# Kernel tuning notes

Measured on AMD Instinct MI355X. Metric: run time of the kernel, lower is better.

## Reference

```python
import jax, jax.numpy as jnp
import numpy as np

TOPK = 10
NUM_CLASSES = 80
ALPHA = 1.0
BETA = 6.0
EPS = 1e-9
IOU_EPS = 1e-7
IMG = 640.0


def setup_inputs() -> dict:
    key = jax.random.key(0)
    ks = jax.random.split(key, 8)
    B, N, M, C = 8, 16800, 96, NUM_CLASSES
    pd_scores = jax.random.normal(ks[0], (B, N, C), dtype=jnp.float32)
    # predicted boxes: valid xyxy around random centers
    p_c = jax.random.uniform(ks[1], (B, N, 2), dtype=jnp.float32) * IMG
    p_wh = jax.random.uniform(ks[2], (B, N, 2), dtype=jnp.float32) * (IMG / 8.0) + 1.0
    pd_bboxes = jnp.concatenate([p_c - p_wh / 2, p_c + p_wh / 2], axis=-1)
    anchor_points = jax.random.uniform(ks[3], (N, 2), dtype=jnp.float32) * IMG
    gt_labels = jax.random.randint(ks[4], (B, M, 1), 0, C, dtype=jnp.int32)
    g_c = jax.random.uniform(ks[5], (B, M, 2), dtype=jnp.float32) * IMG
    g_wh = jax.random.uniform(ks[6], (B, M, 2), dtype=jnp.float32) * (IMG / 4.0) + 4.0
    gt_bboxes = jnp.concatenate([g_c - g_wh / 2, g_c + g_wh / 2], axis=-1)
    # first 72 of 96 GT slots valid per image (padding mask)
    mask_gt = jnp.broadcast_to((jnp.arange(M) < 72).astype(jnp.float32)[None, :, None], (B, M, 1))
    return {"pd_scores": pd_scores, "pd_bboxes": pd_bboxes, "anchor_points": anchor_points,
            "gt_labels": gt_labels, "gt_bboxes": gt_bboxes, "mask_gt": mask_gt}


def _bbox_iou(b1, b2):
    # b1: (B,N,1,4), b2: (B,1,M,4) -> (B,N,M)
    ix1 = jnp.maximum(b1[..., 0], b2[..., 0])
    iy1 = jnp.maximum(b1[..., 1], b2[..., 1])
    ix2 = jnp.minimum(b1[..., 2], b2[..., 2])
    iy2 = jnp.minimum(b1[..., 3], b2[..., 3])
    inter = jnp.clip(ix2 - ix1, 0.0) * jnp.clip(iy2 - iy1, 0.0)
    a1 = (b1[..., 2] - b1[..., 0]) * (b1[..., 3] - b1[..., 1])
    a2 = (b2[..., 2] - b2[..., 0]) * (b2[..., 3] - b2[..., 1])
    return inter / (a1 + a2 - inter + IOU_EPS)


def _assign(pd_scores, pd_bboxes, anchor_points, gt_labels, gt_bboxes, mask_gt):
    B, N, C = pd_scores.shape
    M = gt_bboxes.shape[1]
    mg = mask_gt[:, :, 0]                      # (B,M)
    gl = gt_labels[:, :, 0].astype(jnp.int32)  # (B,M)

    # --- anchor centers inside GT boxes -> (B,N,M) ---
    lt = gt_bboxes[:, :, None, :2]             # (B,M,1,2)
    rb = gt_bboxes[:, :, None, 2:]
    ap = anchor_points[None, None, :, :]       # (1,1,N,2)
    deltas = jnp.concatenate([ap - lt, rb - ap], axis=-1)  # (B,M,N,4)
    mask_in_gts = jnp.swapaxes(deltas.min(-1) > EPS, 1, 2).astype(pd_scores.dtype)  # (B,N,M)

    # --- IoU + alignment metric ---
    overlaps = jnp.clip(_bbox_iou(pd_bboxes[:, :, None, :], gt_bboxes[:, None, :, :]), 0.0)  # (B,N,M)
    gl_exp = jnp.broadcast_to(gl[:, None, :], (B, N, M))
    bbox_scores = jnp.take_along_axis(pd_scores, gl_exp, axis=2)  # (B,N,M)
    align = (jax.nn.sigmoid(bbox_scores) ** ALPHA) * (overlaps ** BETA)
    align = align * mg[:, None, :]

    # --- top-k anchors per GT (over anchor axis) ---
    mT = jnp.swapaxes(align, 1, 2)                     # (B,M,N)
    topk_vals, topk_idxs = jax.lax.top_k(mT, min(TOPK, N))
    keep = topk_vals.max(-1, keepdims=True) > EPS       # (B,M,1)
    bi = jnp.arange(B)[:, None, None]
    mi = jnp.arange(M)[None, :, None]
    sel = jnp.zeros((B, M, N), dtype=bool).at[bi, mi, topk_idxs].set(True)
    mask_topk = jnp.swapaxes(sel & keep, 1, 2).astype(pd_scores.dtype)  # (B,N,M)

    mask_pos = mask_in_gts * mask_topk * mg[:, None, :]

    # --- resolve anchors assigned to multiple GTs by max IoU ---
    fg_count = mask_pos.sum(2)                          # (B,N)
    multi = (fg_count[:, :, None] > 1)
    is_max = jax.nn.one_hot(overlaps.argmax(2), M, dtype=overlaps.dtype)
    mask_pos = jnp.where(multi, is_max, mask_pos)
    fg_mask = mask_pos.sum(2) > 0                       # (B,N) bool
    target_gt_idx = mask_pos.argmax(2)                  # (B,N)

    # --- gather targets ---
    target_labels = jnp.take_along_axis(gl, target_gt_idx, axis=1)
    target_labels = jnp.clip(target_labels, 0, C - 1)
    target_bboxes = jnp.take_along_axis(gt_bboxes, target_gt_idx[:, :, None], axis=1)  # (B,N,4)

    # --- normalized alignment metric -> scores (faithful .long() truncation) ---
    max_per_gt = jnp.clip(align.max(1, keepdims=True), EPS)
    norm_align = (align / max_per_gt).max(2) * fg_mask.astype(align.dtype)  # (B,N)
    bi2 = jnp.arange(B)[:, None]
    ni = jnp.arange(N)[None, :]
    assigned = jnp.zeros((B, N, C), dtype=jnp.int32).at[bi2, ni, target_labels].set(
        norm_align.astype(jnp.int32))
    target_scores = jnp.where(fg_mask[:, :, None], assigned.astype(pd_scores.dtype),
                              jnp.zeros((), pd_scores.dtype))
    return target_bboxes, target_scores, fg_mask, target_gt_idx


def reference(pd_scores, pd_bboxes, anchor_points, gt_labels, gt_bboxes, mask_gt):
    return _assign(pd_scores, pd_bboxes, anchor_points, gt_labels, gt_bboxes, mask_gt)
```

## Files before the change

kernel.cpp:

```cpp
#include <hip/hip_runtime.h>
#include <math.h>

#define TOPK_K 10
#define EPS_F 1e-9f
#define IOU_EPS_F 1e-7f
#define CH 128
#define CCH 256
#define MGMAX 32

struct Iou6 { float ov; float ov6; };

__device__ __forceinline__ Iou6 iou_pow6(float px1, float py1, float px2, float py2,
                                         float gx1, float gy1, float gx2, float gy2) {
#pragma clang fp contract(off)
  float ix1 = fmaxf(px1, gx1);
  float iy1 = fmaxf(py1, gy1);
  float ix2 = fminf(px2, gx2);
  float iy2 = fminf(py2, gy2);
  float dw = fmaxf(ix2 - ix1, 0.0f);
  float dh = fmaxf(iy2 - iy1, 0.0f);
  float inter = dw * dh;
  float a1 = (px2 - px1) * (py2 - py1);
  float a2 = (gx2 - gx1) * (gy2 - gy1);
  float den = a1 + a2 - inter + IOU_EPS_F;
  float iou = inter / den;
  float ov = fmaxf(iou, 0.0f);
  float ov2 = ov * ov;
  Iou6 r; r.ov = ov; r.ov6 = ov2 * ov2 * ov2;
  return r;
}

__device__ __forceinline__ float sigmoid_f(float x) {
#pragma clang fp contract(off)
  return 1.0f / (1.0f + expf(-x));
}

__device__ __forceinline__ unsigned long long mk_key(float v, int idx) {
  if (idx < 0) return 0ull;
  unsigned uv = __float_as_uint(v) | 0x80000000u;
  return ((unsigned long long)uv << 32) | (unsigned)(~idx);
}

#define KINSERT(kk)                                                      \
  if ((kk) > kl[9]) {                                                    \
    _Pragma("unroll")                                                    \
    for (int j = 9; j >= 1; --j) {                                       \
      if ((kk) > kl[j - 1])      kl[j] = kl[j - 1];                      \
      else if ((kk) > kl[j])     kl[j] = (kk);                           \
    }                                                                    \
    if ((kk) > kl[0]) kl[0] = (kk);                                      \
  }

#define WAVE_MERGE10()                                                         \
  {                                                                            \
    _Pragma("unroll")                                                          \
    for (int r = 0; r < TOPK_K; ++r) {                                         \
      unsigned long long kmine = kl[0], kw = kl[0];                            \
      _Pragma("unroll")                                                        \
      for (int off = 32; off > 0; off >>= 1) {                                 \
        unsigned long long o = __shfl_xor(kw, off);                            \
        if (o > kw) kw = o;                                                    \
      }                                                                        \
      if (lane == 0) skey[wid * TOPK_K + r] = kw;                              \
      if (kmine == kw && kw != 0ull) {                  \
        _Pragma("unroll")                                                      \
        for (int j = 0; j < TOPK_K - 1; ++j) kl[j] = kl[j + 1];                \
        kl[TOPK_K - 1] = 0ull;                                                 \
      }                                                                        \
    }                                                                          \
  }

#define FINAL_MERGE10()                                                        \
  {                                                                            \
    _Pragma("unroll")                                                          \
    for (int r = 0; r < TOPK_K; ++r) {                                         \
      unsigned long long kmine = kl[0], kw = kl[0];                            \
      _Pragma("unroll")                                                        \
      for (int off = 32; off > 0; off >>= 1) {                                 \
        unsigned long long o = __shfl_xor(kw, off);                            \
        if (o > kw) kw = o;                                                    \
      }                                                                        \
      if (r == 0) maxv = __uint_as_float((unsigned)(kw >> 32) & 0x7fffffffu);  \
      if (r == TOPK_K - 1) {                                                   \
        Tv = __uint_as_float((unsigned)(kw >> 32) & 0x7fffffffu);              \
        Ti = (int)~(unsigned)(kw & 0xffffffffu);                               \
      }                                                                        \
      if (kmine == kw && kw != 0ull) {                                         \
        _Pragma("unroll")                                                      \
        for (int j = 0; j < TOPK_K - 1; ++j) kl[j] = kl[j + 1];                \
        kl[TOPK_K - 1] = 0ull;                                                 \
      }                                                                        \
    }                                                                          \
  }

__launch_bounds__(256)
__global__ void k_zero(int* __restrict__ cnt, int n) {
  for (int i = threadIdx.x; i < n; i += 256) cnt[i] = 0;
}

__launch_bounds__(CCH)
__global__ void k_collect(const float* __restrict__ pd_scores,
                          const float* __restrict__ pd_bboxes,
                          const int*   __restrict__ gt_labels,
                          const float* __restrict__ gt_bboxes,
                          const float* __restrict__ mask_gt,
                          int B, int N, int M, int C, int CAP, int MGS,
                          int*    __restrict__ cnt,
                          float2* __restrict__ lists)
{
  const int b = blockIdx.z;
  const int m0 = blockIdx.y * MGS;
  const int mcount = min(MGS, M - m0);
  const int tid = threadIdx.x;
  const int n = blockIdx.x * CCH + tid;
  const int lane = tid & 63;
  const int wid  = tid >> 6;

  __shared__ float4             sgt[MGMAX];
  __shared__ int                sgl[MGMAX];
  __shared__ int                smg[MGMAX];
  __shared__ unsigned long long sbal[CCH / 64][MGMAX];
  __shared__ int                wbase[CCH / 64][MGMAX];

  if (tid < mcount) {
    sgt[tid] = *(const float4*)(gt_bboxes + (size_t)(b * M + m0 + tid) * 4);
    sgl[tid] = min(max(gt_labels[b * M + m0 + tid], 0), C - 1);
    smg[tid] = (mask_gt[b * M + m0 + tid] > 0.0f) ? 1 : 0;
  }
  __syncthreads();

  float4 p = make_float4(-1.f, -1.f, -2.f, -2.f);
  if (n < N) p = *(const float4*)(pd_bboxes + ((size_t)b * N + n) * 4);

  for (int mi = 0; mi < mcount; ++mi) {
    const float4 g = sgt[mi];
    bool pred = false;
    if (smg[mi]) {
      float ix1 = fmaxf(p.x, g.x), iy1 = fmaxf(p.y, g.y);
      float ix2 = fminf(p.z, g.z), iy2 = fminf(p.w, g.w);
      pred = (ix2 > ix1) && (iy2 > iy1);
    }
    unsigned long long bal = __ballot(pred);
    if (lane == 0) sbal[wid][mi] = bal;
  }
  __syncthreads();

  if (tid < mcount) {
    int t0 = __popcll(sbal[0][tid]), t1 = __popcll(sbal[1][tid]);
    int t2 = __popcll(sbal[2][tid]), t3 = __popcll(sbal[3][tid]);
    int tot = t0 + t1 + t2 + t3;
    int gb = (tot > 0) ? atomicAdd(&cnt[b * M + m0 + tid], tot) : 0;
    wbase[0][tid] = gb;
    wbase[1][tid] = gb + t0;
    wbase[2][tid] = gb + t0 + t1;
    wbase[3][tid] = gb + t0 + t1 + t2;
  }
  __syncthreads();

  const float* __restrict__ srow = pd_scores + ((size_t)b * N + n) * C;
  const unsigned long long ltm = (1ull << lane) - 1ull;
  for (int mi = 0; mi < mcount; ++mi) {
    unsigned long long bal = sbal[wid][mi];
    if (bal == 0ull) continue;
    if ((bal >> lane) & 1ull) {
      int pos = wbase[wid][mi] + __popcll(bal & ltm);
      if ((unsigned)pos < (unsigned)CAP) {
        const float4 g = sgt[mi];
        Iou6 io = iou_pow6(p.x, p.y, p.z, p.w, g.x, g.y, g.z, g.w);
        float a = sigmoid_f(srow[sgl[mi]]) * io.ov6;
        lists[(size_t)(b * M + m0 + mi) * CAP + pos] = make_float2(a, __int_as_float(n));
      }
    }
  }
}

__launch_bounds__(256)
__global__ void k_select(const float* __restrict__ pd_scores,
                         const float* __restrict__ pd_bboxes,
                         const int*   __restrict__ gt_labels,
                         const float* __restrict__ gt_bboxes,
                         const float* __restrict__ mask_gt,
                         int B, int N, int M, int C, int CAP,
                         const int*    __restrict__ cnt,
                         const float2* __restrict__ lists,
                         float* __restrict__ maxv_out,
                         float* __restrict__ t10v_out,
                         int*   __restrict__ t10i_out)
{
  const int m = blockIdx.x, b = blockIdx.y;
  const int bm = b * M + m;
  const int tid = threadIdx.x;
  const int lane = tid & 63;
  const int wid  = tid >> 6;

  __shared__ unsigned long long skey[4 * TOPK_K];
  __shared__ int sfb;

  if (mask_gt[bm] == 0.0f) {
    if (tid == 0) { maxv_out[bm] = 0.0f; t10v_out[bm] = 0.0f; t10i_out[bm] = -1; }
    return;
  }

  unsigned long long kl[TOPK_K];
#pragma unroll
  for (int j = 0; j < TOPK_K; ++j) kl[j] = 0ull;

  float maxv = 0.0f, Tv = 0.0f; int Ti = -1;
  const int c = cnt[bm];
  bool fb = (c < TOPK_K) || (c > CAP);

  if (!fb) {
    const float2* __restrict__ lp = lists + (size_t)bm * CAP;
    for (int i = tid; i < c; i += 256) {
      float2 e = lp[i];
      unsigned long long k = mk_key(e.x, __float_as_int(e.y));
      KINSERT(k);
    }
    WAVE_MERGE10();
    __syncthreads();
    if (wid == 0) {
#pragma unroll
      for (int j = 0; j < TOPK_K; ++j) kl[j] = 0ull;
      kl[0] = (lane < 4 * TOPK_K) ? skey[lane] : 0ull;
      FINAL_MERGE10();
      if (lane == 0) sfb = (Tv == 0.0f) ? 1 : 0;
    }
    __syncthreads();
    fb = (sfb != 0);
  }

  if (fb) {
#pragma unroll
    for (int j = 0; j < TOPK_K; ++j) kl[j] = 0ull;
    const float4 g = *(const float4*)(gt_bboxes + (size_t)bm * 4);
    int gl = min(max(gt_labels[bm], 0), C - 1);
    const float* __restrict__ srow = pd_scores + (size_t)b * N * C;
    const float4* __restrict__ pb = (const float4*)(pd_bboxes + (size_t)b * N * 4);
    for (int n = tid; n < N; n += 256) {
      float4 p = pb[n];
      Iou6 io = iou_pow6(p.x, p.y, p.z, p.w, g.x, g.y, g.z, g.w);
      unsigned long long kub = mk_key(io.ov6, 0);
      if (kub > kl[TOPK_K - 1]) {
        float a = (io.ov6 == 0.0f) ? 0.0f
                                   : sigmoid_f(srow[(size_t)n * C + gl]) * io.ov6;
        unsigned long long k = mk_key(a, n);
        KINSERT(k);
      }
    }
    __syncthreads();
    WAVE_MERGE10();
    __syncthreads();
    if (wid == 0) {
#pragma unroll
      for (int j = 0; j < TOPK_K; ++j) kl[j] = 0ull;
      kl[0] = (lane < 4 * TOPK_K) ? skey[lane] : 0ull;
      FINAL_MERGE10();
    }
  }

  if (tid == 0) { maxv_out[bm] = maxv; t10v_out[bm] = Tv; t10i_out[bm] = Ti; }
}

__launch_bounds__(256)
__global__ void k_assign(const float* __restrict__ pd_scores,
                         const float* __restrict__ pd_bboxes,
                         const float* __restrict__ anchors,
                         const int*   __restrict__ gt_labels,
                         const float* __restrict__ gt_bboxes,
                         const float* __restrict__ mask_gt,
                         const float* __restrict__ maxv_in,
                         const float* __restrict__ t10v_in,
                         const int*   __restrict__ t10i_in,
                         int B, int N, int M, int C,
                         float* __restrict__ out)
{
  const int b = blockIdx.y;
  const int chunk0 = blockIdx.x * CH;
  const int tid = threadIdx.x;
  const int al   = tid & (CH - 1);
  const int half = tid >> 7;
  const int n = chunk0 + al;

  __shared__ float4 sgt[128];
  __shared__ int    sgl[128];
  __shared__ float  smg[128];
  __shared__ float  smpg[128];
  __shared__ float  spre[128];
  __shared__ float  smT[128];
  __shared__ int    smI[128];
  __shared__ int    skeep[128];
  __shared__ float  s_pov[CH];
  __shared__ int    s_parg[CH], s_pcnt[CH], s_pfirst[CH], s_pone[CH];
  __shared__ int    slab[CH];
  __shared__ float  ssv[CH];

  if (tid < M) {
    sgt[tid] = *(const float4*)(gt_bboxes + (size_t)(b * M + tid) * 4);
    sgl[tid] = min(max(gt_labels[b * M + tid], 0), C - 1);
    smg[tid] = mask_gt[b * M + tid];
    float mv  = maxv_in[b * M + tid];
    float mpg = fmaxf(mv, EPS_F);
    smpg[tid] = mpg;
    spre[tid] = mpg * 0.999999f;
    smT[tid]  = t10v_in[b * M + tid];
    smI[tid]  = t10i_in[b * M + tid];
    skeep[tid] = (mv > EPS_F) ? 1 : 0;
  }
  __syncthreads();

  float* __restrict__ out_bbox   = out;
  float* __restrict__ out_scores = out + (size_t)B * N * 4;
  float* __restrict__ out_fg     = out_scores + (size_t)B * N * C;
  float* __restrict__ out_tgt    = out_fg + (size_t)B * N;

  const bool valid = (n < N);
  float pov = -1.0f; int parg = 0;
  int pcnt = 0, pfirst = -1, pone = 0;

  if (valid) {
    const float4 p = *(const float4*)(pd_bboxes + ((size_t)b * N + n) * 4);
    const float ax = anchors[(size_t)n * 2];
    const float ay = anchors[(size_t)n * 2 + 1];
    const float* __restrict__ srow = pd_scores + ((size_t)b * N + n) * C;

    const int mhalf = (M + 1) >> 1;
    const int mlo = half ? mhalf : 0;
    const int mhi = half ? M : mhalf;

    for (int m = mlo; m < mhi; ++m) {
      const float4 gbb = sgt[m];
      Iou6 io = iou_pow6(p.x, p.y, p.z, p.w, gbb.x, gbb.y, gbb.z, gbb.w);
      if (io.ov > pov) { pov = io.ov; parg = m; }
      const float mgv = smg[m];
      if (mgv > 0.0f) {
        const float T = smT[m];
        const int keep = skeep[m];
        bool mem = false;
        const bool cand = keep && (io.ov6 > T);
        if (cand || (io.ov6 >= spre[m])) {
          const float a = sigmoid_f(srow[sgl[m]]) * io.ov6;
          if (cand) mem = (a > T) || (a == T && n <= smI[m]);
          if (a / smpg[m] >= 1.0f) pone = 1;
        } else if (keep && (T == 0.0f) && (io.ov6 == 0.0f)) {
          mem = (n <= smI[m]);
        }
        if (mem) {
          const float d = fminf(fminf(ax - gbb.x, ay - gbb.y),
                                fminf(gbb.z - ax, gbb.w - ay));
          if (d > EPS_F) { pcnt++; if (pfirst < 0) pfirst = m; }
        }
      }
    }
  }

  if (half == 1 && valid) {
    s_pov[al] = pov; s_parg[al] = parg; s_pcnt[al] = pcnt;
    s_pfirst[al] = pfirst; s_pone[al] = pone;
  }
  __syncthreads();

  if (half == 0 && valid) {
    float ov1 = s_pov[al];
    if (ov1 > pov) { pov = ov1; parg = s_parg[al]; }
    pcnt += s_pcnt[al];
    if (pfirst < 0) pfirst = s_pfirst[al];
    pone |= s_pone[al];

    float fg; int tgt;
    if (pcnt > 1)       { fg = 1.0f; tgt = parg; }
    else if (pcnt == 1) { fg = 1.0f; tgt = pfirst; }
    else                { fg = 0.0f; tgt = 0; }

    slab[al] = sgl[tgt];
    ssv[al]  = (fg > 0.0f && pone) ? 1.0f : 0.0f;

    *(float4*)(out_bbox + ((size_t)b * N + n) * 4) = sgt[tgt];
    out_fg[(size_t)b * N + n]  = fg;
    out_tgt[(size_t)b * N + n] = (float)tgt;
  }
  __syncthreads();

  const int rows = min(CH, N - chunk0);
  const int c4n = C >> 2;
  float4* __restrict__ os4 = (float4*)(out_scores + ((size_t)b * N + chunk0) * C);
  const int tot = rows * c4n;
  if (c4n == 20) {
    for (int i = tid; i < tot; i += 256) {
      unsigned row = __umulhi((unsigned)i, 0xCCCCCCCDu) >> 4;
      int c0 = (i - (int)row * 20) * 4;
      int lr = slab[row]; float v = ssv[row];
      float4 o;
      o.x = (c0     == lr) ? v : 0.0f;
      o.y = (c0 + 1 == lr) ? v : 0.0f;
      o.z = (c0 + 2 == lr) ? v : 0.0f;
      o.w = (c0 + 3 == lr) ? v : 0.0f;
      os4[i] = o;
    }
  } else {
    for (int i = tid; i < tot; i += 256) {
      int row = i / c4n;
      int c0 = (i - row * c4n) * 4;
      int lr = slab[row]; float v = ssv[row];
      float4 o;
      o.x = (c0     == lr) ? v : 0.0f;
      o.y = (c0 + 1 == lr) ? v : 0.0f;
      o.z = (c0 + 2 == lr) ? v : 0.0f;
      o.w = (c0 + 3 == lr) ? v : 0.0f;
      os4[i] = o;
    }
  }
}

extern "C" void kernel_launch(void* const* d_in, const int* in_sizes, int n_in,
                              void* d_out, int out_size, void* d_ws, size_t ws_size,
                              hipStream_t stream) {
  const float* pd_scores = (const float*)d_in[0];
  const float* pd_bboxes = (const float*)d_in[1];
  const float* anchors   = (const float*)d_in[2];
  const int*   gt_labels = (const int*)d_in[3];
  const float* gt_bboxes = (const float*)d_in[4];
  const float* mask_gt   = (const float*)d_in[5];

  const int N = in_sizes[2] / 2;
  const int B = in_sizes[1] / (N * 4);
  const int M = in_sizes[3] / B;
  const int C = in_sizes[0] / (B * N);
  const int BM = B * M;

  char* ws = (char*)d_ws;
  float*  maxv  = (float*)ws;  ws += (size_t)BM * 4;
  float*  t10v  = (float*)ws;  ws += (size_t)BM * 4;
  int*    t10i  = (int*)ws;    ws += (size_t)BM * 4;
  int*    cnt   = (int*)ws;    ws += (size_t)BM * 4;
  float2* lists = (float2*)ws;

  const size_t header = (size_t)BM * 16;
  size_t avail = (ws_size > header) ? (ws_size - header) : 0;
  long long capll = (long long)(avail / ((size_t)BM * 8));
  int CAP = (int)((capll > 4096) ? 4096 : capll);
  if (CAP < 512) CAP = 0;

  k_zero<<<1, 256, 0, stream>>>(cnt, BM);

  if (CAP > 0) {
    int MGRP = 8;
    int MGS  = (M + MGRP - 1) / MGRP;
    while (MGS > MGMAX) { MGRP *= 2; MGS = (M + MGRP - 1) / MGRP; }
    dim3 gc((N + CCH - 1) / CCH, MGRP, B);
    k_collect<<<gc, CCH, 0, stream>>>(pd_scores, pd_bboxes, gt_labels, gt_bboxes,
                                      mask_gt, B, N, M, C, CAP, MGS, cnt, lists);
  }

  dim3 gs(M, B);
  k_select<<<gs, 256, 0, stream>>>(pd_scores, pd_bboxes, gt_labels, gt_bboxes,
                                   mask_gt, B, N, M, C, CAP, cnt, lists,
                                   maxv, t10v, t10i);

  dim3 g2((N + CH - 1) / CH, B);
  k_assign<<<g2, 256, 0, stream>>>(pd_scores, pd_bboxes, anchors, gt_labels,
                                   gt_bboxes, mask_gt, maxv, t10v, t10i,
                                   B, N, M, C, (float*)d_out);
}
```

Measured before the change: 80.59 us.

## Defer score gathers from collect to select using IoU-bound pruning threshold

The collect kernel now stores only the IoU^6 overlap per candidate and no longer gathers class scores from pd_scores. The select kernel first finds the top-10 candidates by overlap, computes their true alignment values, and takes the minimum as a lower bound L. It then gathers scores only for candidates whose overlap is at least L, since sigmoid is at most one. This cuts the scattered pd_scores reads to a few per GT, at the cost of an extra pass over each list plus a warp merge in select.

```diff
diff --git a/kernel.cpp b/kernel.cpp
--- a/kernel.cpp
+++ b/kernel.cpp
@@ -99,12 +99,10 @@
 }
 
 __launch_bounds__(CCH)
-__global__ void k_collect(const float* __restrict__ pd_scores,
-                          const float* __restrict__ pd_bboxes,
-                          const int*   __restrict__ gt_labels,
+__global__ void k_collect(const float* __restrict__ pd_bboxes,
                           const float* __restrict__ gt_bboxes,
                           const float* __restrict__ mask_gt,
-                          int B, int N, int M, int C, int CAP, int MGS,
+                          int B, int N, int M, int CAP, int MGS,
                           int*    __restrict__ cnt,
                           float2* __restrict__ lists)
 {
@@ -117,14 +115,12 @@
   const int wid  = tid >> 6;
 
   __shared__ float4             sgt[MGMAX];
-  __shared__ int                sgl[MGMAX];
   __shared__ int                smg[MGMAX];
   __shared__ unsigned long long sbal[CCH / 64][MGMAX];
   __shared__ int                wbase[CCH / 64][MGMAX];
 
   if (tid < mcount) {
     sgt[tid] = *(const float4*)(gt_bboxes + (size_t)(b * M + m0 + tid) * 4);
-    sgl[tid] = min(max(gt_labels[b * M + m0 + tid], 0), C - 1);
     smg[tid] = (mask_gt[b * M + m0 + tid] > 0.0f) ? 1 : 0;
   }
   __syncthreads();
@@ -157,7 +153,6 @@
   }
   __syncthreads();
 
-  const float* __restrict__ srow = pd_scores + ((size_t)b * N + n) * C;
   const unsigned long long ltm = (1ull << lane) - 1ull;
   for (int mi = 0; mi < mcount; ++mi) {
     unsigned long long bal = sbal[wid][mi];
@@ -167,8 +162,7 @@
       if ((unsigned)pos < (unsigned)CAP) {
         const float4 g = sgt[mi];
         Iou6 io = iou_pow6(p.x, p.y, p.z, p.w, g.x, g.y, g.z, g.w);
-        float a = sigmoid_f(srow[sgl[mi]]) * io.ov6;
-        lists[(size_t)(b * M + m0 + mi) * CAP + pos] = make_float2(a, __int_as_float(n));
+        lists[(size_t)(b * M + m0 + mi) * CAP + pos] = make_float2(io.ov6, __int_as_float(n));
       }
     }
   }
@@ -194,6 +188,7 @@
   const int wid  = tid >> 6;
 
   __shared__ unsigned long long skey[4 * TOPK_K];
+  __shared__ float sL;
   __shared__ int sfb;
 
   if (mask_gt[bm] == 0.0f) {
@@ -201,6 +196,9 @@
     return;
   }
 
+  const int gl = min(max(gt_labels[bm], 0), C - 1);
+  const float* __restrict__ srow = pd_scores + (size_t)b * N * C;
+
   unsigned long long kl[TOPK_K];
 #pragma unroll
   for (int j = 0; j < TOPK_K; ++j) kl[j] = 0ull;
@@ -211,6 +209,7 @@
 
   if (!fb) {
     const float2* __restrict__ lp = lists + (size_t)bm * CAP;
+
     for (int i = tid; i < c; i += 256) {
       float2 e = lp[i];
       unsigned long long k = mk_key(e.x, __float_as_int(e.y));
@@ -218,6 +217,54 @@
     }
     WAVE_MERGE10();
     __syncthreads();
+
+    if (wid == 0) {
+#pragma unroll
+      for (int j = 0; j < TOPK_K; ++j) kl[j] = 0ull;
+      kl[0] = (lane < 4 * TOPK_K) ? skey[lane] : 0ull;
+      unsigned long long win = 0ull;
+#pragma unroll
+      for (int r = 0; r < TOPK_K; ++r) {
+        unsigned long long kmine = kl[0], kw = kl[0];
+#pragma unroll
+        for (int off = 32; off > 0; off >>= 1) {
+          unsigned long long o = __shfl_xor(kw, off);
+          if (o > kw) kw = o;
+        }
+        if (lane == r) win = kw;
+        if (kmine == kw && kw != 0ull) {
+#pragma unroll
+          for (int j = 0; j < TOPK_K - 1; ++j) kl[j] = kl[j + 1];
+          kl[TOPK_K - 1] = 0ull;
+        }
+      }
+      float al = INFINITY;
+      if (lane < TOPK_K && win != 0ull) {
+        float v = __uint_as_float((unsigned)(win >> 32) & 0x7fffffffu);
+        int wn = (int)~(unsigned)(win & 0xffffffffu);
+        al = sigmoid_f(srow[(size_t)wn * C + gl]) * v;
+      }
+#pragma unroll
+      for (int off = 8; off > 0; off >>= 1)
+        al = fminf(al, __shfl_xor(al, off));
+      if (lane == 0) sL = al;
+    }
+    __syncthreads();
+    const float L = sL;
+
+#pragma unroll
+    for (int j = 0; j < TOPK_K; ++j) kl[j] = 0ull;
+    for (int i = tid; i < c; i += 256) {
+      float2 e = lp[i];
+      if (e.x >= L) {
+        int nn = __float_as_int(e.y);
+        float a = sigmoid_f(srow[(size_t)nn * C + gl]) * e.x;
+        unsigned long long k = mk_key(a, nn);
+        KINSERT(k);
+      }
+    }
+    WAVE_MERGE10();
+    __syncthreads();
     if (wid == 0) {
 #pragma unroll
       for (int j = 0; j < TOPK_K; ++j) kl[j] = 0ull;
@@ -233,8 +280,6 @@
 #pragma unroll
     for (int j = 0; j < TOPK_K; ++j) kl[j] = 0ull;
     const float4 g = *(const float4*)(gt_bboxes + (size_t)bm * 4);
-    int gl = min(max(gt_labels[bm], 0), C - 1);
-    const float* __restrict__ srow = pd_scores + (size_t)b * N * C;
     const float4* __restrict__ pb = (const float4*)(pd_bboxes + (size_t)b * N * 4);
     for (int n = tid; n < N; n += 256) {
       float4 p = pb[n];
@@ -447,8 +492,8 @@
     int MGS  = (M + MGRP - 1) / MGRP;
     while (MGS > MGMAX) { MGRP *= 2; MGS = (M + MGRP - 1) / MGRP; }
     dim3 gc((N + CCH - 1) / CCH, MGRP, B);
-    k_collect<<<gc, CCH, 0, stream>>>(pd_scores, pd_bboxes, gt_labels, gt_bboxes,
-                                      mask_gt, B, N, M, C, CAP, MGS, cnt, lists);
+    k_collect<<<gc, CCH, 0, stream>>>(pd_bboxes, gt_bboxes, mask_gt,
+                                      B, N, M, CAP, MGS, cnt, lists);
   }
 
   dim3 gs(M, B);
```

After: 85.76 us. 1.06x slower.

## Stage per-GT candidates in shared memory with LDS atomics before coalesced global write

Applied to the files above, without the earlier changes.

The collect kernel no longer uses two passes of wave ballots. Each thread now computes the alignment metric inline and appends it into a per-GT shared-memory staging buffer through LDS atomics. One global atomic per GT reserves space, and the block then writes the staged entries out contiguously for coalesced stores. GT groups shrink to 12 per block, and an overflow flag makes the select kernel fall back to the slow path when the staging or global capacity is exceeded. This removes the scattered global writes, at the cost of shared-memory atomic contention and a serial linear search to find each entry's GT.

```diff
diff --git a/kernel.cpp b/kernel.cpp
--- a/kernel.cpp
+++ b/kernel.cpp
@@ -6,7 +6,8 @@
 #define IOU_EPS_F 1e-7f
 #define CH 128
 #define CCH 256
-#define MGMAX 32
+#define MG 12
+#define SCAP 96
 
 struct Iou6 { float ov; float ov6; };
 
@@ -94,8 +95,8 @@
   }
 
 __launch_bounds__(256)
-__global__ void k_zero(int* __restrict__ cnt, int n) {
-  for (int i = threadIdx.x; i < n; i += 256) cnt[i] = 0;
+__global__ void k_zero(int* __restrict__ p, int n) {
+  for (int i = blockIdx.x * 256 + threadIdx.x; i < n; i += gridDim.x * 256) p[i] = 0;
 }
 
 __launch_bounds__(CCH)
@@ -104,73 +105,79 @@
                           const int*   __restrict__ gt_labels,
                           const float* __restrict__ gt_bboxes,
                           const float* __restrict__ mask_gt,
-                          int B, int N, int M, int C, int CAP, int MGS,
+                          int B, int N, int M, int C, int CAP,
                           int*    __restrict__ cnt,
+                          int*    __restrict__ ovf,
                           float2* __restrict__ lists)
 {
   const int b = blockIdx.z;
-  const int m0 = blockIdx.y * MGS;
-  const int mcount = min(MGS, M - m0);
+  const int m0 = blockIdx.y * MG;
+  const int mcount = min(MG, M - m0);
   const int tid = threadIdx.x;
   const int n = blockIdx.x * CCH + tid;
-  const int lane = tid & 63;
-  const int wid  = tid >> 6;
-
-  __shared__ float4             sgt[MGMAX];
-  __shared__ int                sgl[MGMAX];
-  __shared__ int                smg[MGMAX];
-  __shared__ unsigned long long sbal[CCH / 64][MGMAX];
-  __shared__ int                wbase[CCH / 64][MGMAX];
+
+  __shared__ float4 sgt[MG];
+  __shared__ int    sgl[MG];
+  __shared__ int    smg[MG];
+  __shared__ int    scnt[MG];
+  __shared__ int    sgb[MG];
+  __shared__ int    swr[MG];
+  __shared__ int    sstart[MG];
+  __shared__ int    stotal;
+  __shared__ float2 stage[MG][SCAP];
 
   if (tid < mcount) {
     sgt[tid] = *(const float4*)(gt_bboxes + (size_t)(b * M + m0 + tid) * 4);
     sgl[tid] = min(max(gt_labels[b * M + m0 + tid], 0), C - 1);
     smg[tid] = (mask_gt[b * M + m0 + tid] > 0.0f) ? 1 : 0;
+    scnt[tid] = 0;
   }
   __syncthreads();
 
   float4 p = make_float4(-1.f, -1.f, -2.f, -2.f);
   if (n < N) p = *(const float4*)(pd_bboxes + ((size_t)b * N + n) * 4);
+  const float* __restrict__ srow = pd_scores + ((size_t)b * N + n) * C;
 
   for (int mi = 0; mi < mcount; ++mi) {
+    if (!smg[mi]) continue;
     const float4 g = sgt[mi];
-    bool pred = false;
-    if (smg[mi]) {
-      float ix1 = fmaxf(p.x, g.x), iy1 = fmaxf(p.y, g.y);
-      float ix2 = fminf(p.z, g.z), iy2 = fminf(p.w, g.w);
-      pred = (ix2 > ix1) && (iy2 > iy1);
-    }
-    unsigned long long bal = __ballot(pred);
-    if (lane == 0) sbal[wid][mi] = bal;
+    float ix1 = fmaxf(p.x, g.x), iy1 = fmaxf(p.y, g.y);
+    float ix2 = fminf(p.z, g.z), iy2 = fminf(p.w, g.w);
+    if (ix2 > ix1 && iy2 > iy1) {
+      Iou6 io = iou_pow6(p.x, p.y, p.z, p.w, g.x, g.y, g.z, g.w);
+      float a = sigmoid_f(srow[sgl[mi]]) * io.ov6;
+      int pos = atomicAdd(&scnt[mi], 1);
+      if (pos < SCAP) stage[mi][pos] = make_float2(a, __int_as_float(n));
+    }
   }
   __syncthreads();
 
   if (tid < mcount) {
-    int t0 = __popcll(sbal[0][tid]), t1 = __popcll(sbal[1][tid]);
-    int t2 = __popcll(sbal[2][tid]), t3 = __popcll(sbal[3][tid]);
-    int tot = t0 + t1 + t2 + t3;
-    int gb = (tot > 0) ? atomicAdd(&cnt[b * M + m0 + tid], tot) : 0;
-    wbase[0][tid] = gb;
-    wbase[1][tid] = gb + t0;
-    wbase[2][tid] = gb + t0 + t1;
-    wbase[3][tid] = gb + t0 + t1 + t2;
-  }
-  __syncthreads();
-
-  const float* __restrict__ srow = pd_scores + ((size_t)b * N + n) * C;
-  const unsigned long long ltm = (1ull << lane) - 1ull;
-  for (int mi = 0; mi < mcount; ++mi) {
-    unsigned long long bal = sbal[wid][mi];
-    if (bal == 0ull) continue;
-    if ((bal >> lane) & 1ull) {
-      int pos = wbase[wid][mi] + __popcll(bal & ltm);
-      if ((unsigned)pos < (unsigned)CAP) {
-        const float4 g = sgt[mi];
-        Iou6 io = iou_pow6(p.x, p.y, p.z, p.w, g.x, g.y, g.z, g.w);
-        float a = sigmoid_f(srow[sgl[mi]]) * io.ov6;
-        lists[(size_t)(b * M + m0 + mi) * CAP + pos] = make_float2(a, __int_as_float(n));
-      }
-    }
+    int c = scnt[tid];
+    int w = min(c, SCAP);
+    int gb = 0;
+    if (w > 0) {
+      gb = atomicAdd(&cnt[b * M + m0 + tid], w);
+      if (gb + w > CAP) { atomicOr(&ovf[b * M + m0 + tid], 1); w = max(0, CAP - gb); }
+    }
+    if (c > SCAP) atomicOr(&ovf[b * M + m0 + tid], 1);
+    sgb[tid] = gb;
+    swr[tid] = w;
+  }
+  __syncthreads();
+  if (tid == 0) {
+    int acc = 0;
+    for (int mi = 0; mi < mcount; ++mi) { sstart[mi] = acc; acc += swr[mi]; }
+    stotal = acc;
+  }
+  __syncthreads();
+
+  const int tot = stotal;
+  for (int i = tid; i < tot; i += CCH) {
+    int mi = 0;
+    while (mi + 1 < mcount && i >= sstart[mi + 1]) ++mi;
+    int off = i - sstart[mi];
+    lists[(size_t)(b * M + m0 + mi) * CAP + sgb[mi] + off] = stage[mi][off];
   }
 }
 
@@ -182,6 +189,7 @@
                          const float* __restrict__ mask_gt,
                          int B, int N, int M, int C, int CAP,
                          const int*    __restrict__ cnt,
+                         const int*    __restrict__ ovf,
                          const float2* __restrict__ lists,
                          float* __restrict__ maxv_out,
                          float* __restrict__ t10v_out,
@@ -207,7 +215,7 @@
 
   float maxv = 0.0f, Tv = 0.0f; int Ti = -1;
   const int c = cnt[bm];
-  bool fb = (c < TOPK_K) || (c > CAP);
+  bool fb = (c < TOPK_K) || (c > CAP) || (ovf[bm] != 0);
 
   if (!fb) {
     const float2* __restrict__ lp = lists + (size_t)bm * CAP;
@@ -432,28 +440,29 @@
   float*  t10v  = (float*)ws;  ws += (size_t)BM * 4;
   int*    t10i  = (int*)ws;    ws += (size_t)BM * 4;
   int*    cnt   = (int*)ws;    ws += (size_t)BM * 4;
+  int*    ovf   = (int*)ws;    ws += (size_t)BM * 4;
   float2* lists = (float2*)ws;
 
-  const size_t header = (size_t)BM * 16;
+  const size_t header = (size_t)BM * 20;
   size_t avail = (ws_size > header) ? (ws_size - header) : 0;
   long long capll = (long long)(avail / ((size_t)BM * 8));
   int CAP = (int)((capll > 4096) ? 4096 : capll);
   if (CAP < 512) CAP = 0;
 
-  k_zero<<<1, 256, 0, stream>>>(cnt, BM);
+  k_zero<<<2, 256, 0, stream>>>(cnt, BM * 2);
 
   if (CAP > 0) {
-    int MGRP = 8;
-    int MGS  = (M + MGRP - 1) / MGRP;
-    while (MGS > MGMAX) { MGRP *= 2; MGS = (M + MGRP - 1) / MGRP; }
+    const int MGRP = (M + MG - 1) / MG;
     dim3 gc((N + CCH - 1) / CCH, MGRP, B);
     k_collect<<<gc, CCH, 0, stream>>>(pd_scores, pd_bboxes, gt_labels, gt_bboxes,
-                                      mask_gt, B, N, M, C, CAP, MGS, cnt, lists);
+                                      mask_gt, B, N, M, C, CAP, cnt, ovf, lists);
+  } else {
+    k_zero<<<1, 256, 0, stream>>>(cnt, BM);
   }
 
   dim3 gs(M, B);
   k_select<<<gs, 256, 0, stream>>>(pd_scores, pd_bboxes, gt_labels, gt_bboxes,
-                                   mask_gt, B, N, M, C, CAP, cnt, lists,
+                                   mask_gt, B, N, M, C, CAP, cnt, ovf, lists,
                                    maxv, t10v, t10i);
 
   dim3 g2((N + CH - 1) / CH, B);
```

New measurement: 77.93 us. -3.3%, faster.
